# Kernel tuning notes

Hardware: AMD Instinct MI355X
Metric: run time of the kernel (lower is better)

Reference implementation:

```python
import jax, jax.numpy as jnp
import numpy as np
from functools import partial

B, H, W = 2, 480, 480
C, HALF = 32, 16
L, WN, PAD = 4, 20, 20

def gelu(x):
    return jax.nn.gelu(x, approximate=False)

def setup_inputs() -> dict:
    key = jax.random.key(0)
    ks = jax.random.split(key, 24)
    scale = 1.0 / (C * C)
    d = {}
    d["input_data"] = jax.random.normal(ks[0], (B, H, W, 1), jnp.float32)
    d["src_data"] = jax.random.normal(ks[1], (B, H, W, 3), jnp.float32)
    # input lifting MLP: sizes [5, 16, 32]
    d["in_w1"] = jax.random.normal(ks[2], (5, HALF), jnp.float32) * 0.1
    d["in_b1"] = jnp.zeros((HALF,), jnp.float32)
    d["in_w2"] = jax.random.normal(ks[3], (HALF, C), jnp.float32) * 0.1
    d["in_b2"] = jnp.zeros((C,), jnp.float32)
    # eps lifting MLP: sizes [3, 16, 32]
    d["eps_w1"] = jax.random.normal(ks[4], (3, HALF), jnp.float32) * 0.1
    d["eps_b1"] = jnp.zeros((HALF,), jnp.float32)
    d["eps_w2"] = jax.random.normal(ks[5], (HALF, C), jnp.float32) * 0.1
    d["eps_b2"] = jnp.zeros((C,), jnp.float32)
    # Fourier layer params, stacked over L layers
    d["fw1"] = jax.random.uniform(ks[6], (L, C, C, WN, WN, 2), jnp.float32) * scale
    d["fw2"] = jax.random.uniform(ks[7], (L, C, C, WN, WN, 2), jnp.float32) * scale
    d["conv_w"] = jax.random.normal(ks[8], (L, C, C), jnp.float32) * 0.05
    d["conv_b"] = jnp.zeros((L, C), jnp.float32)
    # projection MLP: sizes [32, 16, 2]
    d["proj_w1"] = jax.random.normal(ks[9], (C, HALF), jnp.float32) * 0.1
    d["proj_b1"] = jnp.zeros((HALF,), jnp.float32)
    d["proj_w2"] = jax.random.normal(ks[10], (HALF, 2), jnp.float32) * 0.1
    d["proj_b2"] = jnp.zeros((2,), jnp.float32)
    # mask conv 3x3, 1->1 channel
    d["mask_w"] = jax.random.normal(ks[11], (1, 1, 3, 3), jnp.float32) * 0.1
    d["mask_b"] = jnp.zeros((1,), jnp.float32)
    return d

def _grid(b, h, w):
    gx = jnp.broadcast_to(jnp.linspace(0.0, 1.0, h, dtype=jnp.float32)[None, :, None, None], (b, h, w, 1))
    gy = jnp.broadcast_to(jnp.linspace(0.0, 1.0, w, dtype=jnp.float32)[None, None, :, None], (b, h, w, 1))
    return jnp.concatenate([gx, gy], axis=-1)

def _mlp(x, w1, b1, w2, b2):
    # FCLayer(gelu) then FCLayer(linear)
    return gelu(x @ w1 + b1) @ w2 + b2

def _fourier_conv(x, x_eps, w1, w2):
    # x, x_eps: [B, C, Hp, Wp]
    hp, wp = x.shape[-2], x.shape[-1]
    xf = jnp.fft.rfft2(x * x_eps)                       # [B,C,Hp,Wp//2+1] complex
    xr = jnp.stack([xf.real, xf.imag], axis=-1)         # [B,C,Hp,Wp//2+1,2]
    lo = jnp.einsum('bixyz,ioxyz->boxyz', xr[:, :, :WN, :WN, :], w1)
    hi = jnp.einsum('bixyz,ioxyz->boxyz', xr[:, :, -WN:, :WN, :], w2)
    out = jnp.zeros((x.shape[0], w1.shape[1], hp, wp // 2 + 1, 2), jnp.float32)
    out = out.at[:, :, :WN, :WN, :].set(lo)
    out = out.at[:, :, -WN:, :WN, :].set(hi)
    return jnp.fft.irfft2(out[..., 0] + 1j * out[..., 1], s=(hp, wp))

def _forward(input_data, src_data, in_w1, in_b1, in_w2, in_b2,
             eps_w1, eps_b1, eps_w2, eps_b2, fw1, fw2, conv_w, conv_b,
             proj_w1, proj_b1, proj_w2, proj_b2, mask_w, mask_b):
    b, h, w = input_data.shape[0], input_data.shape[1], input_data.shape[2]
    grid = _grid(b, h, w)
    x_in = jnp.concatenate([src_data, grid], axis=-1)       # [B,H,W,5]
    x_eps = jnp.concatenate([input_data, grid], axis=-1)    # [B,H,W,3]
    field = src_data[..., 1:]                               # [B,H,W,2]

    a = _mlp(x_in, in_w1, in_b1, in_w2, in_b2)              # [B,H,W,C]
    a = jnp.transpose(a, (0, 3, 1, 2))                      # [B,C,H,W]
    a = jnp.pad(a, ((0, 0), (0, 0), (0, PAD), (0, PAD)))    # [B,C,H+P,W+P]
    e = _mlp(x_eps, eps_w1, eps_b1, eps_w2, eps_b2)
    e = jnp.transpose(e, (0, 3, 1, 2))
    e = jnp.pad(e, ((0, 0), (0, 0), (0, PAD), (0, PAD)))

    for l in range(L):
        x1 = _fourier_conv(a, e, fw1[l], fw2[l])
        x2 = jnp.einsum('bihw,oi->bohw', a, conv_w[l]) + conv_b[l][None, :, None, None]
        a = x1 + x2
        if l < L - 1:
            a = gelu(a)

    pred = a[..., :-PAD, :-PAD]                             # [B,C,H,W]
    pred = jnp.transpose(pred, (0, 2, 3, 1))                # [B,H,W,C]
    pred = _mlp(pred, proj_w1, proj_b1, proj_w2, proj_b2)   # [B,H,W,2]

    xm = jnp.transpose(input_data, (0, 3, 1, 2))            # [B,1,H,W]
    mask = jax.lax.conv_general_dilated(xm, mask_w, (1, 1), 'SAME',
                                        dimension_numbers=('NCHW', 'OIHW', 'NCHW'))
    mask = mask + mask_b[None, :, None, None]
    mask = jnp.transpose(mask, (0, 2, 3, 1))                # [B,H,W,1] -> broadcasts over 2
    return field * mask + pred

def reference(input_data, src_data, in_w1, in_b1, in_w2, in_b2,
              eps_w1, eps_b1, eps_w2, eps_b2, fw1, fw2, conv_w, conv_b,
              proj_w1, proj_b1, proj_w2, proj_b2, mask_w, mask_b):
    return _forward(input_data, src_data, in_w1, in_b1, in_w2, in_b2,
                    eps_w1, eps_b1, eps_w2, eps_b2, fw1, fw2, conv_w, conv_b,
                    proj_w1, proj_b1, proj_w2, proj_b2, mask_w, mask_b)
```

## Files before the change

kernel.cpp:

```cpp
#include <hip/hip_runtime.h>
#include <hip/hip_bf16.h>

#define BD 2
#define HD 480
#define WD 480
#define CD 32
#define HALFD 16
#define WND 20
#define NP 500
#define PLANE (HD*WD)
#define TWO_PI_OVER_NP 0.012566370614359172954f

typedef __attribute__((ext_vector_type(8))) short bf16x8;
typedef __attribute__((ext_vector_type(4))) float f32x4;

__device__ __forceinline__ float gelu_f(float x) {
    return 0.5f * x * (1.0f + erff(x * 0.70710678118654752f));
}
__device__ __forceinline__ float bfbits2f(short s) {
    unsigned u = ((unsigned)(unsigned short)s) << 16;
    return __uint_as_float(u);
}
__device__ __forceinline__ short bf16s(float v) {
    __hip_bfloat16 b = __float2bfloat16(v);
    return *reinterpret_cast<short*>(&b);
}
__device__ __forceinline__ unsigned pk2(float a, float b) {
    return (unsigned)(unsigned short)bf16s(a) | ((unsigned)(unsigned short)bf16s(b) << 16);
}

__global__ void __launch_bounds__(256) k_ae(
    const float* src, const float* inp,
    const float* iw1, const float* ib1,
    const float* iw2, const float* ib2,
    const float* ew1, const float* eb1,
    const float* ew2, const float* eb2,
    __hip_bfloat16* A, __hip_bfloat16* E)
{
    __shared__ float s_iw1[80], s_ib1[16];
    __shared__ float s_ew1[48], s_eb1[16];
    __shared__ __align__(16) __hip_bfloat16 s_hidA[256 * 24];
    __shared__ __align__(16) __hip_bfloat16 s_hidE[256 * 24];
    __shared__ __align__(16) __hip_bfloat16 s_out[32 * 264];

    int tid = threadIdx.x;
    int lane = tid & 63, wv = tid >> 6;

    if (tid < 80) s_iw1[tid] = iw1[tid];
    if (tid >= 96 && tid < 112) s_ib1[tid - 96] = ib1[tid - 96];
    if (tid >= 128 && tid < 176) s_ew1[tid - 128] = ew1[tid - 128];
    if (tid >= 192 && tid < 208) s_eb1[tid - 192] = eb1[tid - 192];

    int c0 = lane & 15, kg = lane >> 4;
    bf16x8 bIn[2], bEps[2];
    float biasIn[2], biasEps[2];
    #pragma unroll
    for (int nt = 0; nt < 2; nt++) {
        int c = nt * 16 + c0;
        #pragma unroll
        for (int j = 0; j < 8; j++) {
            int k = kg * 8 + j;
            bIn[nt][j]  = (k < 16) ? bf16s(iw2[k * 32 + c]) : (short)0;
            bEps[nt][j] = (k < 16) ? bf16s(ew2[k * 32 + c]) : (short)0;
        }
        biasIn[nt]  = ib2[c];
        biasEps[nt] = eb2[c];
    }
    __syncthreads();

    int gid = blockIdx.x * 256 + tid;
    int b = gid / PLANE;
    int r = gid % PLANE;
    int h = r / WD, w = r % WD;
    float gx = (float)h * (1.0f / 479.0f);
    float gy = (float)w * (1.0f / 479.0f);
    float s0 = src[(size_t)gid * 3 + 0];
    float s1 = src[(size_t)gid * 3 + 1];
    float s2 = src[(size_t)gid * 3 + 2];
    float xi = inp[gid];

    {
        unsigned pk[8];
        #pragma unroll
        for (int j = 0; j < 16; j += 2) {
            float v0 = s_ib1[j]     + s0 * s_iw1[j]     + s1 * s_iw1[16 + j]
                     + s2 * s_iw1[32 + j]     + gx * s_iw1[48 + j]     + gy * s_iw1[64 + j];
            float v1 = s_ib1[j + 1] + s0 * s_iw1[j + 1] + s1 * s_iw1[16 + j + 1]
                     + s2 * s_iw1[32 + j + 1] + gx * s_iw1[48 + j + 1] + gy * s_iw1[64 + j + 1];
            pk[j >> 1] = pk2(gelu_f(v0), gelu_f(v1));
        }
        uint4* d = reinterpret_cast<uint4*>(&s_hidA[tid * 24]);
        d[0] = make_uint4(pk[0], pk[1], pk[2], pk[3]);
        d[1] = make_uint4(pk[4], pk[5], pk[6], pk[7]);
        #pragma unroll
        for (int j = 0; j < 16; j += 2) {
            float v0 = s_eb1[j]     + xi * s_ew1[j]     + gx * s_ew1[16 + j]     + gy * s_ew1[32 + j];
            float v1 = s_eb1[j + 1] + xi * s_ew1[j + 1] + gx * s_ew1[16 + j + 1] + gy * s_ew1[32 + j + 1];
            pk[j >> 1] = pk2(gelu_f(v0), gelu_f(v1));
        }
        uint4* d2 = reinterpret_cast<uint4*>(&s_hidE[tid * 24]);
        d2[0] = make_uint4(pk[0], pk[1], pk[2], pk[3]);
        d2[1] = make_uint4(pk[4], pk[5], pk[6], pk[7]);
    }
    __syncthreads();

    int r0 = (blockIdx.x % 900) * 256;

    #pragma unroll
    for (int pass = 0; pass < 2; pass++) {
        const __hip_bfloat16* hid = pass ? s_hidE : s_hidA;
        #pragma unroll
        for (int t = 0; t < 4; t++) {
            int tile = wv * 4 + t;
            bf16x8 av = {0, 0, 0, 0, 0, 0, 0, 0};
            if (kg < 2)
                av = *reinterpret_cast<const bf16x8*>(&hid[(tile * 16 + c0) * 24 + kg * 8]);
            #pragma unroll
            for (int nt = 0; nt < 2; nt++) {
                f32x4 acc = {0.f, 0.f, 0.f, 0.f};
                bf16x8 bv = pass ? bEps[nt] : bIn[nt];
                acc = __builtin_amdgcn_mfma_f32_16x16x32_bf16(av, bv, acc, 0, 0, 0);
                float bias = pass ? biasEps[nt] : biasIn[nt];
                int ch = nt * 16 + c0;
                int px = tile * 16 + kg * 4;
                unsigned w0 = pk2(acc[0] + bias, acc[1] + bias);
                unsigned w1 = pk2(acc[2] + bias, acc[3] + bias);
                *reinterpret_cast<uint2*>(&s_out[ch * 264 + px]) = make_uint2(w0, w1);
            }
        }
        __syncthreads();
        __hip_bfloat16* dst = (pass ? E : A) + (size_t)b * CD * PLANE + r0;
        #pragma unroll
        for (int i = 0; i < 4; i++) {
            int idx = tid + i * 256;
            int ch = idx >> 5, chunk = idx & 31;
            uint4 v = *reinterpret_cast<const uint4*>(&s_out[ch * 264 + chunk * 8]);
            *reinterpret_cast<uint4*>(&dst[(size_t)ch * PLANE + chunk * 8]) = v;
        }
        __syncthreads();
    }
}

__global__ void k_tables(__hip_bfloat16* T) {
    int e = blockIdx.x * 256 + threadIdx.x;
    if (e >= 435 * 512) return;
    int tile = e >> 9, r = e & 511;
    int lane = r >> 3, j = r & 7;
    float v = 0.0f;
    if (tile < 45) {
        int kt = tile / 3, nt = tile % 3;
        int k = kt * 32 + ((lane >> 4) << 3) + j;
        int n = nt * 16 + (lane & 15);
        if (n < 40) {
            int ky = n >> 1;
            int idx = (k * ky) % NP;
            float ang = (float)idx * TWO_PI_OVER_NP;
            v = (n & 1) ? -sinf(ang) : cosf(ang);
        }
    } else if (tile < 105) {
        int t2 = tile - 45;
        int nt = t2 >> 1, kt = t2 & 1;
        int kk = kt * 32 + ((lane >> 4) << 3) + j;
        int w = nt * 16 + (lane & 15);
        if (kk < 40) {
            int ky = kk >> 1;
            int idx = (ky * w) % NP;
            float ang = (float)idx * TWO_PI_OVER_NP;
            v = (kk & 1) ? -sinf(ang) : cosf(ang);
        }
    } else if (tile < 255) {
        int t2 = tile - 105;
        int kt = t2 / 5, nt = t2 % 5;
        int k = kt * 32 + ((lane >> 4) << 3) + j;
        int n = nt * 16 + (lane & 15);
        int hh = k >> 1, ri = k & 1;
        int kxi = n >> 1, part = n & 1;
        int kx = (kxi < 20) ? kxi : kxi + 460;
        int idx = (kx * hh) % NP;
        float ang = (float)idx * TWO_PI_OVER_NP;
        float c = cosf(ang), s = sinf(ang);
        v = (part == 0) ? (ri == 0 ? c : s) : (ri == 0 ? -s : c);
    } else {
        int t2 = tile - 255;
        int nt = t2 / 3, kt = t2 % 3;
        int k = kt * 32 + ((lane >> 4) << 3) + j;
        int n = nt * 16 + (lane & 15);
        if (k < 80) {
            int kxi = k >> 1, ri = k & 1;
            int hh = n >> 1, part = n & 1;
            int kx = (kxi < 20) ? kxi : kxi + 460;
            int idx = (kx * hh) % NP;
            float ang = (float)idx * TWO_PI_OVER_NP;
            float c = cosf(ang), s = sinf(ang);
            v = (part == 0) ? (ri == 0 ? c : -s) : (ri == 0 ? s : c);
        }
    }
    T[e] = __float2bfloat16(v);
}

__global__ void __launch_bounds__(256) k_F1m(
    const __hip_bfloat16* A, const __hip_bfloat16* E,
    const __hip_bfloat16* Twig, __hip_bfloat16* Y1)
{
    int wv = threadIdx.x >> 6, lane = threadIdx.x & 63;
    int task = blockIdx.x * 4 + wv;
    int bh = task / 6, rem = task % 6;
    int mt = rem & 1, nt = rem >> 1;
    int b = bh / HD, h = bh % HD;
    int c = mt * 16 + (lane & 15);
    int koff = (lane >> 4) << 3;
    size_t base = ((size_t)(b * 32 + c)) * PLANE + (size_t)h * WD + koff;
    const __hip_bfloat16* arow = A + base;
    const __hip_bfloat16* erow = E + base;
    f32x4 acc = {0.f, 0.f, 0.f, 0.f};
    #pragma unroll
    for (int kt = 0; kt < 15; kt++) {
        bf16x8 av = *reinterpret_cast<const bf16x8*>(arow + kt * 32);
        bf16x8 ev = *reinterpret_cast<const bf16x8*>(erow + kt * 32);
        bf16x8 gv;
        #pragma unroll
        for (int j = 0; j < 8; j++)
            gv[j] = bf16s(bfbits2f(av[j]) * bfbits2f(ev[j]));
        bf16x8 bv = *reinterpret_cast<const bf16x8*>(Twig + (((kt * 3 + nt) << 9) + lane * 8));
        acc = __builtin_amdgcn_mfma_f32_16x16x32_bf16(gv, bv, acc, 0, 0, 0);
    }
    int n = nt * 16 + (lane & 15);
    if (n < 40) {
        int ky = n >> 1, part = n & 1;
        int crow = mt * 16 + ((lane >> 4) << 2);
        #pragma unroll
        for (int r = 0; r < 4; r++) {
            int cc = crow + r;
            Y1[((((size_t)(b * 32 + cc)) * WND + ky) * HD + h) * 2 + part] =
                __float2bfloat16(acc[r]);
        }
    }
}

__global__ void __launch_bounds__(64) k_F2m(
    const __hip_bfloat16* Y1, const __hip_bfloat16* Tf2, float* Y2)
{
    int lane = threadIdx.x;
    int task = blockIdx.x;
    int mt = task / 5, nt = task % 5;
    int row = mt * 16 + (lane & 15);
    int koff = (lane >> 4) << 3;
    const __hip_bfloat16* arow = Y1 + (size_t)row * 960 + koff;
    f32x4 acc = {0.f, 0.f, 0.f, 0.f};
    #pragma unroll
    for (int kt = 0; kt < 30; kt++) {
        bf16x8 av = *reinterpret_cast<const bf16x8*>(arow + kt * 32);
        bf16x8 bv = *reinterpret_cast<const bf16x8*>(Tf2 + (((kt * 5 + nt) << 9) + lane * 8));
        acc = __builtin_amdgcn_mfma_f32_16x16x32_bf16(av, bv, acc, 0, 0, 0);
    }
    int n = nt * 16 + (lane & 15);
    int mb = mt * 16 + ((lane >> 4) << 2);
    #pragma unroll
    for (int r = 0; r < 4; r++)
        Y2[(size_t)(mb + r) * 80 + n] = acc[r];
}

__global__ void __launch_bounds__(256) k_mix(
    const float* Y2, __hip_bfloat16* Zb,
    const float* fw1, const float* fw2, int l)
{
    int gid = blockIdx.x * 256 + threadIdx.x;
    int col = gid % 96;
    int row = gid / 96;
    if (col >= 80) { Zb[gid] = __float2bfloat16(0.0f); return; }
    int ky = row % 20;
    int oc = (row / 20) % 32;
    int b = row / 640;
    int z = col & 1;
    int kxi = col >> 1;
    const float* wp;
    int x;
    if (kxi < 20) { wp = fw1; x = kxi; } else { wp = fw2; x = kxi - 20; }
    size_t wbase = ((((size_t)(l * 32) * 32 + oc) * 20 + x) * 20 + ky) * 2 + z;
    const float* y2 = Y2 + ((size_t)b * 32 * 20 + ky) * 80 + kxi * 2 + z;
    float acc = 0.f;
    for (int i = 0; i < 32; i++) {
        float yv = y2[(size_t)i * 1600];
        float wv = wp[wbase + (size_t)i * 25600];
        acc += yv * wv;
    }
    Zb[gid] = __float2bfloat16(acc);
}

__global__ void __launch_bounds__(256) k_I1m(
    const __hip_bfloat16* Zb, const __hip_bfloat16* Ti1, __hip_bfloat16* U)
{
    int wv = threadIdx.x >> 6, lane = threadIdx.x & 63;
    int task = blockIdx.x * 4 + wv;
    int mt = task / 60, nt = task % 60;
    int row = mt * 16 + (lane & 15);
    int koff = (lane >> 4) << 3;
    const __hip_bfloat16* arow = Zb + (size_t)row * 96 + koff;
    f32x4 acc = {0.f, 0.f, 0.f, 0.f};
    #pragma unroll
    for (int kt = 0; kt < 3; kt++) {
        bf16x8 av = *reinterpret_cast<const bf16x8*>(arow + kt * 32);
        bf16x8 bv = *reinterpret_cast<const bf16x8*>(Ti1 + (((nt * 3 + kt) << 9) + lane * 8));
        acc = __builtin_amdgcn_mfma_f32_16x16x32_bf16(av, bv, acc, 0, 0, 0);
    }
    int n = nt * 16 + (lane & 15);
    int mb = mt * 16 + ((lane >> 4) << 2);
    #pragma unroll
    for (int r = 0; r < 4; r++)
        U[(size_t)(mb + r) * 960 + n] = __float2bfloat16(acc[r]);
}

__global__ void __launch_bounds__(512) k_I2F1(
    const __hip_bfloat16* U, __hip_bfloat16* A,
    const __hip_bfloat16* E,
    const float* convw, const float* convb,
    const __hip_bfloat16* TinvF, const __hip_bfloat16* Twig,
    __hip_bfloat16* Y1, int l)
{
    __shared__ __align__(16) __hip_bfloat16 sUf[4 * 512];
    __shared__ __align__(16) __hip_bfloat16 sWf[2 * 512];
    __shared__ __align__(16) __hip_bfloat16 sA[32 * 488];
    __shared__ float sB[CD];
    int tid = threadIdx.x;
    int b = blockIdx.x / HD;
    int h = blockIdx.x % HD;
    if (tid < CD) sB[tid] = convb[l * CD + tid];
    for (int t = tid; t < 2048; t += 512) {
        int j = t & 7, lane = (t >> 3) & 63, ktmt = t >> 9;
        int mt = ktmt >> 1, kt = ktmt & 1;
        int oc = mt * 16 + (lane & 15);
        int kk = kt * 32 + ((lane >> 4) << 3) + j;
        float v = 0.f;
        if (kk < 40) {
            int ky = kk >> 1;
            __hip_bfloat162 u = reinterpret_cast<const __hip_bfloat162*>(U)
                [(((size_t)b * CD + oc) * WND + ky) * HD + h];
            float sc = (ky == 0 ? 1.0f : 2.0f) * (1.0f / 250000.0f);
            v = ((kk & 1) ? __bfloat162float(u.y) : __bfloat162float(u.x)) * sc;
        }
        sUf[t] = __float2bfloat16(v);
    }
    for (int t = tid; t < 1024; t += 512) {
        int j = t & 7, lane = (t >> 3) & 63, mt = t >> 9;
        int oc = mt * 16 + (lane & 15);
        int ic = ((lane >> 4) << 3) + j;
        sWf[t] = __float2bfloat16(convw[(size_t)l * CD * CD + oc * CD + ic]);
    }
    __syncthreads();
    int wv = tid >> 6, lane = tid & 63;
    int c0 = lane & 15, kg = lane >> 4;
    const unsigned short* Ap = reinterpret_cast<const unsigned short*>(A)
        + (size_t)b * CD * PLANE + (size_t)h * WD;
    for (int t = wv; t < 60; t += 8) {
        int mt = t & 1, nt = t >> 1;
        f32x4 acc = {0.f, 0.f, 0.f, 0.f};
        #pragma unroll
        for (int kt = 0; kt < 2; kt++) {
            bf16x8 av = *reinterpret_cast<const bf16x8*>(&sUf[((mt * 2 + kt) << 9) + lane * 8]);
            bf16x8 bv = *reinterpret_cast<const bf16x8*>(TinvF + (((nt * 2 + kt) << 9) + lane * 8));
            acc = __builtin_amdgcn_mfma_f32_16x16x32_bf16(av, bv, acc, 0, 0, 0);
        }
        bf16x8 av2 = *reinterpret_cast<const bf16x8*>(&sWf[(mt << 9) + lane * 8]);
        bf16x8 bv2;
        #pragma unroll
        for (int j = 0; j < 8; j++)
            bv2[j] = (short)Ap[(size_t)(kg * 8 + j) * PLANE + nt * 16 + c0];
        acc = __builtin_amdgcn_mfma_f32_16x16x32_bf16(av2, bv2, acc, 0, 0, 0);
        int w = nt * 16 + c0;
        int ocb = mt * 16 + (kg << 2);
        #pragma unroll
        for (int r = 0; r < 4; r++) {
            short sv = bf16s(gelu_f(acc[r] + sB[ocb + r]));
            sA[(ocb + r) * 488 + w] = *reinterpret_cast<__hip_bfloat16*>(&sv);
        }
    }
    __syncthreads();
    {
        __hip_bfloat16* Adst = A + (size_t)b * CD * PLANE + (size_t)h * WD;
        for (int t = tid; t < 32 * 60; t += 512) {
            int row = t / 60, chunk = t % 60;
            uint4 v = *reinterpret_cast<const uint4*>(&sA[row * 488 + chunk * 8]);
            *reinterpret_cast<uint4*>(&Adst[(size_t)row * PLANE + chunk * 8]) = v;
        }
    }
    for (int t = wv; t < 6; t += 8) {
        int mt = t & 1, nt = t >> 1;
        int c = mt * 16 + c0;
        const __hip_bfloat16* erow =
            E + ((size_t)(b * 32 + c)) * PLANE + (size_t)h * WD + (kg << 3);
        const __hip_bfloat16* albase = &sA[c * 488 + (kg << 3)];
        f32x4 acc = {0.f, 0.f, 0.f, 0.f};
        #pragma unroll
        for (int kt = 0; kt < 15; kt++) {
            bf16x8 av = *reinterpret_cast<const bf16x8*>(albase + kt * 32);
            bf16x8 ev = *reinterpret_cast<const bf16x8*>(erow + kt * 32);
            bf16x8 gv;
            #pragma unroll
            for (int j = 0; j < 8; j++)
                gv[j] = bf16s(bfbits2f(av[j]) * bfbits2f(ev[j]));
            bf16x8 bv = *reinterpret_cast<const bf16x8*>(Twig + (((kt * 3 + nt) << 9) + lane * 8));
            acc = __builtin_amdgcn_mfma_f32_16x16x32_bf16(gv, bv, acc, 0, 0, 0);
        }
        int n = nt * 16 + c0;
        if (n < 40) {
            int ky = n >> 1, part = n & 1;
            int crow = mt * 16 + (kg << 2);
            #pragma unroll
            for (int r = 0; r < 4; r++) {
                int cc = crow + r;
                Y1[((((size_t)(b * 32 + cc)) * WND + ky) * HD + h) * 2 + part] =
                    __float2bfloat16(acc[r]);
            }
        }
    }
}

__global__ void __launch_bounds__(512) k_I2out(
    const __hip_bfloat16* U, const __hip_bfloat16* A,
    const float* convw, const float* convb,
    const __hip_bfloat16* TinvF,
    const float* inp, const float* src,
    const float* pw1, const float* pb1,
    const float* pw2, const float* pb2,
    const float* mw, const float* mb,
    float* out, int l)
{
    __shared__ __align__(16) __hip_bfloat16 sUf[4 * 512];
    __shared__ __align__(16) __hip_bfloat16 sWf[2 * 512];
    __shared__ __hip_bfloat16 sAT[WD * 33];
    __shared__ float sB[CD];
    __shared__ float sW1[CD * HALFD], sB1[HALFD], sW2[HALFD * 2], sB2[2], sM[9], sMB[1];
    int tid = threadIdx.x;
    int b = blockIdx.x / HD;
    int h = blockIdx.x % HD;
    if (tid < CD) sB[tid] = convb[l * CD + tid];
    sW1[tid] = pw1[tid];
    if (tid >= 32 && tid < 48) sB1[tid - 32] = pb1[tid - 32];
    if (tid >= 64 && tid < 96) sW2[tid - 64] = pw2[tid - 64];
    if (tid >= 96 && tid < 98) sB2[tid - 96] = pb2[tid - 96];
    if (tid >= 128 && tid < 137) sM[tid - 128] = mw[tid - 128];
    if (tid == 160) sMB[0] = mb[0];
    for (int t = tid; t < 2048; t += 512) {
        int j = t & 7, lane = (t >> 3) & 63, ktmt = t >> 9;
        int mt = ktmt >> 1, kt = ktmt & 1;
        int oc = mt * 16 + (lane & 15);
        int kk = kt * 32 + ((lane >> 4) << 3) + j;
        float v = 0.f;
        if (kk < 40) {
            int ky = kk >> 1;
            __hip_bfloat162 u = reinterpret_cast<const __hip_bfloat162*>(U)
                [(((size_t)b * CD + oc) * WND + ky) * HD + h];
            float sc = (ky == 0 ? 1.0f : 2.0f) * (1.0f / 250000.0f);
            v = ((kk & 1) ? __bfloat162float(u.y) : __bfloat162float(u.x)) * sc;
        }
        sUf[t] = __float2bfloat16(v);
    }
    for (int t = tid; t < 1024; t += 512) {
        int j = t & 7, lane = (t >> 3) & 63, mt = t >> 9;
        int oc = mt * 16 + (lane & 15);
        int ic = ((lane >> 4) << 3) + j;
        sWf[t] = __float2bfloat16(convw[(size_t)l * CD * CD + oc * CD + ic]);
    }
    __syncthreads();
    int wv = tid >> 6, lane = tid & 63;
    int c0 = lane & 15, kg = lane >> 4;
    const unsigned short* Ap = reinterpret_cast<const unsigned short*>(A)
        + (size_t)b * CD * PLANE + (size_t)h * WD;
    for (int t = wv; t < 60; t += 8) {
        int mt = t & 1, nt = t >> 1;
        f32x4 acc = {0.f, 0.f, 0.f, 0.f};
        #pragma unroll
        for (int kt = 0; kt < 2; kt++) {
            bf16x8 av = *reinterpret_cast<const bf16x8*>(&sUf[((mt * 2 + kt) << 9) + lane * 8]);
            bf16x8 bv = *reinterpret_cast<const bf16x8*>(TinvF + (((nt * 2 + kt) << 9) + lane * 8));
            acc = __builtin_amdgcn_mfma_f32_16x16x32_bf16(av, bv, acc, 0, 0, 0);
        }
        bf16x8 av2 = *reinterpret_cast<const bf16x8*>(&sWf[(mt << 9) + lane * 8]);
        bf16x8 bv2;
        #pragma unroll
        for (int j = 0; j < 8; j++)
            bv2[j] = (short)Ap[(size_t)(kg * 8 + j) * PLANE + nt * 16 + c0];
        acc = __builtin_amdgcn_mfma_f32_16x16x32_bf16(av2, bv2, acc, 0, 0, 0);
        int w = nt * 16 + c0;
        int ocb = mt * 16 + (kg << 2);
        #pragma unroll
        for (int r = 0; r < 4; r++) {
            short sv = bf16s(acc[r] + sB[ocb + r]);
            sAT[w * 33 + (ocb + r)] = *reinterpret_cast<__hip_bfloat16*>(&sv);
        }
    }
    __syncthreads();
    for (int w = tid; w < WD; w += 512) {
        float av[32];
        #pragma unroll
        for (int i = 0; i < 32; i++) av[i] = bfbits2f(
            *reinterpret_cast<const short*>(&sAT[w * 33 + i]));
        float hid[16];
        #pragma unroll
        for (int j = 0; j < 16; j++) {
            float v = sB1[j];
            #pragma unroll
            for (int i = 0; i < 32; i++) v += av[i] * sW1[i * 16 + j];
            hid[j] = gelu_f(v);
        }
        float p0 = sB2[0], p1 = sB2[1];
        #pragma unroll
        for (int j = 0; j < 16; j++) { p0 += hid[j] * sW2[j * 2]; p1 += hid[j] * sW2[j * 2 + 1]; }
        float m = sMB[0];
        #pragma unroll
        for (int dh = 0; dh < 3; dh++) {
            int hh = h + dh - 1;
            #pragma unroll
            for (int dw = 0; dw < 3; dw++) {
                int ww = w + dw - 1;
                if (hh >= 0 && hh < HD && ww >= 0 && ww < WD)
                    m += inp[(size_t)b * PLANE + (size_t)hh * WD + ww] * sM[dh * 3 + dw];
            }
        }
        size_t gid = (size_t)b * PLANE + (size_t)h * WD + w;
        float f0 = src[gid * 3 + 1];
        float f1 = src[gid * 3 + 2];
        out[gid * 2 + 0] = f0 * m + p0;
        out[gid * 2 + 1] = f1 * m + p1;
    }
}

extern "C" void kernel_launch(void* const* d_in, const int* in_sizes, int n_in,
                              void* d_out, int out_size, void* d_ws, size_t ws_size,
                              hipStream_t stream) {
    const float* inp = (const float*)d_in[0];
    const float* src = (const float*)d_in[1];
    const float* iw1 = (const float*)d_in[2];
    const float* ib1 = (const float*)d_in[3];
    const float* iw2 = (const float*)d_in[4];
    const float* ib2 = (const float*)d_in[5];
    const float* ew1 = (const float*)d_in[6];
    const float* eb1 = (const float*)d_in[7];
    const float* ew2 = (const float*)d_in[8];
    const float* eb2 = (const float*)d_in[9];
    const float* fw1 = (const float*)d_in[10];
    const float* fw2 = (const float*)d_in[11];
    const float* cw  = (const float*)d_in[12];
    const float* cb  = (const float*)d_in[13];
    const float* pw1 = (const float*)d_in[14];
    const float* pb1 = (const float*)d_in[15];
    const float* pw2 = (const float*)d_in[16];
    const float* pb2 = (const float*)d_in[17];
    const float* mw  = (const float*)d_in[18];
    const float* mb  = (const float*)d_in[19];

    const size_t NA = (size_t)BD * CD * PLANE;
    __hip_bfloat16* A   = (__hip_bfloat16*)d_ws;
    __hip_bfloat16* E   = A + NA;
    __hip_bfloat16* Y1U = E + NA;
    float* Y2 = (float*)(Y1U + (size_t)BD * CD * WND * HD * 2);
    __hip_bfloat16* Zb = (__hip_bfloat16*)(Y2 + 1280 * 80);
    __hip_bfloat16* Tbl   = Zb + 1280 * 96;
    __hip_bfloat16* Twig  = Tbl;
    __hip_bfloat16* TinvF = Twig + 45 * 512;
    __hip_bfloat16* Tf2   = TinvF + 60 * 512;
    __hip_bfloat16* Ti1   = Tf2 + 150 * 512;

    k_tables<<<870, 256, 0, stream>>>(Tbl);
    k_ae<<<1800, 256, 0, stream>>>(src, inp, iw1, ib1, iw2, ib2,
                                   ew1, eb1, ew2, eb2, A, E);

    k_F1m<<<1440, 256, 0, stream>>>(A, E, Twig, Y1U);
    for (int l = 0; l < 4; l++) {
        k_F2m<<<400, 64, 0, stream>>>(Y1U, Tf2, Y2);
        k_mix<<<480, 256, 0, stream>>>(Y2, Zb, fw1, fw2, l);
        k_I1m<<<1200, 256, 0, stream>>>(Zb, Ti1, Y1U);
        if (l < 3)
            k_I2F1<<<BD * HD, 512, 0, stream>>>(Y1U, A, E, cw, cb, TinvF, Twig,
                                                Y1U, l);
        else
            k_I2out<<<BD * HD, 512, 0, stream>>>(Y1U, A, cw, cb, TinvF,
                                                 inp, src, pw1, pb1, pw2, pb2,
                                                 mw, mb, (float*)d_out, l);
    }
}
```

Before: 391.3 us.

## Move projection MLP to MFMA and overlap activation store with DFT

Result: faster. 373.4 us (-4.6%).

```diff
diff --git a/kernel.cpp b/kernel.cpp
--- a/kernel.cpp
+++ b/kernel.cpp
@@ -375,16 +375,8 @@
         }
     }
     __syncthreads();
-    {
-        __hip_bfloat16* Adst = A + (size_t)b * CD * PLANE + (size_t)h * WD;
-        for (int t = tid; t < 32 * 60; t += 512) {
-            int row = t / 60, chunk = t % 60;
-            uint4 v = *reinterpret_cast<const uint4*>(&sA[row * 488 + chunk * 8]);
-            *reinterpret_cast<uint4*>(&Adst[(size_t)row * PLANE + chunk * 8]) = v;
-        }
-    }
-    for (int t = wv; t < 6; t += 8) {
-        int mt = t & 1, nt = t >> 1;
+    if (wv < 6) {
+        int mt = wv & 1, nt = wv >> 1;
         int c = mt * 16 + c0;
         const __hip_bfloat16* erow =
             E + ((size_t)(b * 32 + c)) * PLANE + (size_t)h * WD + (kg << 3);
@@ -412,6 +404,13 @@
                     __float2bfloat16(acc[r]);
             }
         }
+    } else {
+        __hip_bfloat16* Adst = A + (size_t)b * CD * PLANE + (size_t)h * WD;
+        for (int t = tid - 384; t < 32 * 60; t += 128) {
+            int row = t / 60, chunk = t % 60;
+            uint4 v = *reinterpret_cast<const uint4*>(&sA[row * 488 + chunk * 8]);
+            *reinterpret_cast<uint4*>(&Adst[(size_t)row * PLANE + chunk * 8]) = v;
+        }
     }
 }
 
@@ -427,24 +426,30 @@
 {
     __shared__ __align__(16) __hip_bfloat16 sUf[4 * 512];
     __shared__ __align__(16) __hip_bfloat16 sWf[2 * 512];
-    __shared__ __hip_bfloat16 sAT[WD * 33];
+    __shared__ __align__(16) __hip_bfloat16 sAT[WD * 40];
+    __shared__ float sP[WD * 2];
     __shared__ float sB[CD];
-    __shared__ float sW1[CD * HALFD], sB1[HALFD], sW2[HALFD * 2], sB2[2], sM[9], sMB[1];
+    __shared__ float sB1[HALFD], sW2[HALFD * 2], sB2[2], sM[9], sMB[1];
     int tid = threadIdx.x;
+    int lane = tid & 63, wv = tid >> 6;
+    int c0 = lane & 15, kg = lane >> 4;
     int b = blockIdx.x / HD;
     int h = blockIdx.x % HD;
     if (tid < CD) sB[tid] = convb[l * CD + tid];
-    sW1[tid] = pw1[tid];
     if (tid >= 32 && tid < 48) sB1[tid - 32] = pb1[tid - 32];
     if (tid >= 64 && tid < 96) sW2[tid - 64] = pw2[tid - 64];
     if (tid >= 96 && tid < 98) sB2[tid - 96] = pb2[tid - 96];
     if (tid >= 128 && tid < 137) sM[tid - 128] = mw[tid - 128];
     if (tid == 160) sMB[0] = mb[0];
+    bf16x8 bW1;
+    #pragma unroll
+    for (int j = 0; j < 8; j++)
+        bW1[j] = bf16s(pw1[(kg * 8 + j) * 16 + c0]);
     for (int t = tid; t < 2048; t += 512) {
-        int j = t & 7, lane = (t >> 3) & 63, ktmt = t >> 9;
+        int j = t & 7, lane2 = (t >> 3) & 63, ktmt = t >> 9;
         int mt = ktmt >> 1, kt = ktmt & 1;
-        int oc = mt * 16 + (lane & 15);
-        int kk = kt * 32 + ((lane >> 4) << 3) + j;
+        int oc = mt * 16 + (lane2 & 15);
+        int kk = kt * 32 + ((lane2 >> 4) << 3) + j;
         float v = 0.f;
         if (kk < 40) {
             int ky = kk >> 1;
@@ -456,14 +461,12 @@
         sUf[t] = __float2bfloat16(v);
     }
     for (int t = tid; t < 1024; t += 512) {
-        int j = t & 7, lane = (t >> 3) & 63, mt = t >> 9;
-        int oc = mt * 16 + (lane & 15);
-        int ic = ((lane >> 4) << 3) + j;
+        int j = t & 7, lane2 = (t >> 3) & 63, mt = t >> 9;
+        int oc = mt * 16 + (lane2 & 15);
+        int ic = ((lane2 >> 4) << 3) + j;
         sWf[t] = __float2bfloat16(convw[(size_t)l * CD * CD + oc * CD + ic]);
     }
     __syncthreads();
-    int wv = tid >> 6, lane = tid & 63;
-    int c0 = lane & 15, kg = lane >> 4;
     const unsigned short* Ap = reinterpret_cast<const unsigned short*>(A)
         + (size_t)b * CD * PLANE + (size_t)h * WD;
     for (int t = wv; t < 60; t += 8) {
@@ -483,29 +486,36 @@
         acc = __builtin_amdgcn_mfma_f32_16x16x32_bf16(av2, bv2, acc, 0, 0, 0);
         int w = nt * 16 + c0;
         int ocb = mt * 16 + (kg << 2);
+        unsigned q0 = pk2(acc[0] + sB[ocb + 0], acc[1] + sB[ocb + 1]);
+        unsigned q1 = pk2(acc[2] + sB[ocb + 2], acc[3] + sB[ocb + 3]);
+        *reinterpret_cast<uint2*>(&sAT[w * 40 + ocb]) = make_uint2(q0, q1);
+    }
+    __syncthreads();
+    for (int t = wv; t < 30; t += 8) {
+        bf16x8 av = *reinterpret_cast<const bf16x8*>(&sAT[(t * 16 + c0) * 40 + kg * 8]);
+        f32x4 acc = {0.f, 0.f, 0.f, 0.f};
+        acc = __builtin_amdgcn_mfma_f32_16x16x32_bf16(av, bW1, acc, 0, 0, 0);
         #pragma unroll
         for (int r = 0; r < 4; r++) {
-            short sv = bf16s(acc[r] + sB[ocb + r]);
-            sAT[w * 33 + (ocb + r)] = *reinterpret_cast<__hip_bfloat16*>(&sv);
+            float hid = gelu_f(acc[r] + sB1[c0]);
+            float p0 = hid * sW2[c0 * 2 + 0];
+            float p1 = hid * sW2[c0 * 2 + 1];
+            #pragma unroll
+            for (int m = 1; m < 16; m <<= 1) {
+                p0 += __shfl_xor(p0, m, 64);
+                p1 += __shfl_xor(p1, m, 64);
+            }
+            if (c0 == 0) {
+                int px = t * 16 + kg * 4 + r;
+                sP[px * 2 + 0] = p0 + sB2[0];
+                sP[px * 2 + 1] = p1 + sB2[1];
+            }
         }
     }
     __syncthreads();
     for (int w = tid; w < WD; w += 512) {
-        float av[32];
-        #pragma unroll
-        for (int i = 0; i < 32; i++) av[i] = bfbits2f(
-            *reinterpret_cast<const short*>(&sAT[w * 33 + i]));
-        float hid[16];
-        #pragma unroll
-        for (int j = 0; j < 16; j++) {
-            float v = sB1[j];
-            #pragma unroll
-            for (int i = 0; i < 32; i++) v += av[i] * sW1[i * 16 + j];
-            hid[j] = gelu_f(v);
-        }
-        float p0 = sB2[0], p1 = sB2[1];
-        #pragma unroll
-        for (int j = 0; j < 16; j++) { p0 += hid[j] * sW2[j * 2]; p1 += hid[j] * sW2[j * 2 + 1]; }
+        float p0 = sP[w * 2 + 0];
+        float p1 = sP[w * 2 + 1];
         float m = sMB[0];
         #pragma unroll
         for (int dh = 0; dh < 3; dh++) {
```
